# Optimization experiments

Hardware: AMD Instinct MI355X
Metric: run time of the kernel (lower is better)

## Reference

```python
import jax, jax.numpy as jnp
import numpy as np

IFZ = 256      # in_features
SFZ = 1280     # sequence_features
AHZ = 8        # attention heads
AFZ = 64       # attention feature dim per head
NRES = 20      # canonical_num_residues
SCALE = float(np.sqrt(AFZ))
RESID = float(np.sqrt(2.0))
EPS = 1e-6


def _ln(x, s, b, eps=1e-5):
    m = jnp.mean(x, axis=-1, keepdims=True)
    v = jnp.var(x, axis=-1, keepdims=True)
    return (x - m) / jnp.sqrt(v + eps) * s + b


def setup_inputs() -> dict:
    key = jax.random.key(0)
    ks = jax.random.split(key, 20)
    N, B, S = 4096, 4, 512
    HD = AHZ * AFZ
    w = lambda k, shp: (jax.random.normal(k, shp, jnp.float32) * 0.02)
    d = {}
    d["x"] = jax.random.normal(ks[0], (N, IFZ), jnp.float32)
    d["packed_sequence_emb"] = jax.random.normal(ks[1], (B, S, SFZ), jnp.float32)
    d["packed_sequence_mask"] = jnp.ones((B, S), jnp.float32)
    d["prot_mask"] = jnp.arange(N, dtype=jnp.int32)
    d["batch"] = jax.random.randint(ks[2], (N,), 0, B, jnp.int32)
    # projections (bias=False)
    d["Wq"] = w(ks[3], (HD, IFZ))
    d["Wk"] = w(ks[4], (HD, SFZ))
    d["Wv"] = w(ks[5], (HD, SFZ))
    # ag: LayerNorm(HD) -> Linear(HD, IFZ, bias=False) (dropout = identity at eval)
    d["ag_ln_s"] = jnp.ones((HD,), jnp.float32)
    d["ag_ln_b"] = jnp.zeros((HD,), jnp.float32)
    d["Wag"] = w(ks[6], (IFZ, HD))
    d["res_ln_s"] = jnp.ones((3, IFZ), jnp.float32)
    d["res_ln_b"] = jnp.zeros((3, IFZ), jnp.float32)
    d["res_w1"] = w(ks[7], (3, IFZ, IFZ))
    d["res_b1"] = jnp.zeros((3, IFZ), jnp.float32)
    d["res_w2"] = w(ks[8], (3, IFZ, IFZ))
    d["res_b2"] = jnp.zeros((3, IFZ), jnp.float32)
    d["head_w"] = w(ks[9], (NRES, IFZ))
    d["head_b"] = jnp.zeros((NRES,), jnp.float32)
    # output LayerNorm en
    d["en_s"] = jnp.ones((IFZ,), jnp.float32)
    d["en_b"] = jnp.zeros((IFZ,), jnp.float32)
    return d


def _forward(x, emb, mask, prot_mask, batch, Wq, Wk, Wv, ag_ln_s, ag_ln_b, Wag,
             res_ln_s, res_ln_b, res_w1, res_b1, res_w2, res_b2,
             head_w, head_b, en_s, en_b):
    N = x.shape[0]
    B, S = emb.shape[:2]
    b_idx = batch[prot_mask]                      # [M]
    xp = x[prot_mask]                             # [M, IFZ]
    M = xp.shape[0]
    q = (xp @ Wq.T).reshape(M, AHZ, AFZ)          # [M,H,D]
    k = (emb @ Wk.T).reshape(B, S, AHZ, AFZ)      # [B,S,H,D]
    v = (emb @ Wv.T).reshape(B, S, AHZ, AFZ)
    # score vs every protein, then pick own protein (avoids materializing [M,S,H,D] gather)
    scores_all = jnp.einsum('mhd,bshd->mbsh', q, k) / SCALE          # [M,B,S,H]
    sel = b_idx[:, None, None, None]
    scores = jnp.take_along_axis(scores_all, sel, axis=1)[:, 0]       # [M,S,H]
    mb = mask[b_idx][:, :, None]                                      # [M,S,1]
    # padded_sequence_softmax: softmax over S, zero pads, renormalize
    sm = jax.nn.softmax(scores, axis=1) * mb
    w = sm / (jnp.sum(sm, axis=1, keepdims=True) + EPS)               # [M,S,H]
    feat_all = jnp.einsum('msh,bshd->mbhd', w, v)                     # [M,B,H,D]
    feat = jnp.take_along_axis(feat_all, sel, axis=1)[:, 0]
    feat = feat.reshape(M, AHZ * AFZ)
    ag = _ln(feat, ag_ln_s, ag_ln_b) @ Wag.T                          # [M, IFZ]
    # seq_aa_head on the scattered new features (identical to ag for unique prot_mask)
    h = ag
    for i in range(3):
        y = _ln(h, res_ln_s[i], res_ln_b[i])
        y = jax.nn.relu(y @ res_w1[i].T + res_b1[i])
        y = y @ res_w2[i].T + res_b2[i]
        h = (h + y) / RESID
    logits = h @ head_w.T + head_b                                     # [M, NRES]
    new_features = jnp.zeros_like(x).at[prot_mask].set(ag)
    seq_aa_logits = jnp.zeros((N, NRES), x.dtype).at[prot_mask].set(logits)
    unpacked_scores = jnp.zeros((N, S, AHZ), x.dtype).at[prot_mask].set(scores)
    out_x = _ln(x + new_features / RESID, en_s, en_b)
    return out_x, seq_aa_logits, unpacked_scores


def reference(x, packed_sequence_emb, packed_sequence_mask, prot_mask, batch,
              Wq, Wk, Wv, ag_ln_s, ag_ln_b, Wag,
              res_ln_s, res_ln_b, res_w1, res_b1, res_w2, res_b2,
              head_w, head_b, en_s, en_b):
    return _forward(x, packed_sequence_emb, packed_sequence_mask, prot_mask, batch,
                    Wq, Wk, Wv, ag_ln_s, ag_ln_b, Wag,
                    res_ln_s, res_ln_b, res_w1, res_b1, res_w2, res_b2,
                    head_w, head_b, en_s, en_b)
```

## Files before the change

### kernel.cpp

```cpp
#include <hip/hip_runtime.h>
#include <math.h>


typedef short bf8 __attribute__((ext_vector_type(8)));
typedef float f32x4 __attribute__((ext_vector_type(4)));
typedef unsigned short u16;

constexpr int LDT = 40;
enum { EPI_NONE = 0, EPI_BIAS_RELU = 1, EPI_BIAS = 2, EPI_RESID = 3 };
#define RSQRT2 0.70710678118654752f

__device__ __forceinline__ u16 f2bf(float f) {
  unsigned int u = __builtin_bit_cast(unsigned int, f);
  unsigned int r = u + 0x7fffu + ((u >> 16) & 1u);
  return (u16)(r >> 16);
}
__device__ __forceinline__ float bf2f(u16 v) {
  return __builtin_bit_cast(float, (unsigned int)v << 16);
}
__device__ __forceinline__ f32x4 mfma16(bf8 a, bf8 b, f32x4 c) {
  return __builtin_amdgcn_mfma_f32_16x16x32_bf16(a, b, c, 0, 0, 0);
}

struct CvtDesc { const float* src; u16* dst; int n; };
struct CvtArgs { CvtDesc d[8]; };

__global__ __launch_bounds__(256) void cvt_k(CvtArgs a) {
  CvtDesc d = a.d[blockIdx.z];
  int i = (blockIdx.x * 256 + threadIdx.x) * 8;
  if (i >= d.n) return;
  f32x4 v0 = *(const f32x4*)(d.src + i);
  f32x4 v1 = *(const f32x4*)(d.src + i + 4);
  bf8 o;
  o[0] = (short)f2bf(v0[0]); o[1] = (short)f2bf(v0[1]);
  o[2] = (short)f2bf(v0[2]); o[3] = (short)f2bf(v0[3]);
  o[4] = (short)f2bf(v1[0]); o[5] = (short)f2bf(v1[1]);
  o[6] = (short)f2bf(v1[2]); o[7] = (short)f2bf(v1[3]);
  *(bf8*)(d.dst + i) = o;
}

template <int EPI, bool BFOUT>
__global__ __launch_bounds__(256) void mgemm2(
    const u16* __restrict__ A, const u16* __restrict__ B,
    void* __restrict__ Cv, int M, int N, int K, int lda, int ldb, int ldc,
    const float* __restrict__ bias, const float* __restrict__ Hin,
    const int* __restrict__ gatherA, const int* __restrict__ scatterC) {
  __shared__ __align__(16) u16 As[128 * LDT];
  __shared__ __align__(16) u16 Bs[64 * LDT];
  const int tid = threadIdx.x;
  const int m0 = blockIdx.y * 128, n0 = blockIdx.x * 64;
  const int wave = tid >> 6, lane = tid & 63;
  const int wm = (wave & 1) * 64, wn = (wave >> 1) * 32;
  const int lrow = lane & 15, quad = lane >> 4;
  const int srow = tid >> 2, skq = tid & 3;

  int gr0 = m0 + srow, gr1 = m0 + srow + 64;
  int ar0 = (gr0 < M) ? (gatherA ? gatherA[gr0] : gr0) : -1;
  int ar1 = (gr1 < M) ? (gatherA ? gatherA[gr1] : gr1) : -1;
  const u16* Ap0 = (ar0 >= 0) ? A + (size_t)ar0 * lda + skq * 8 : nullptr;
  const u16* Ap1 = (ar1 >= 0) ? A + (size_t)ar1 * lda + skq * 8 : nullptr;
  const u16* Bp = (n0 + srow < N) ? B + (size_t)(n0 + srow) * ldb + skq * 8 : nullptr;
  u16* AsW0 = &As[srow * LDT + skq * 8];
  u16* AsW1 = &As[(srow + 64) * LDT + skq * 8];
  u16* BsW = &Bs[srow * LDT + skq * 8];

  f32x4 acc[4][2];
#pragma unroll
  for (int i = 0; i < 4; ++i)
#pragma unroll
    for (int j = 0; j < 2; ++j) acc[i][j] = (f32x4){0.f, 0.f, 0.f, 0.f};
  const bf8 z8 = {0, 0, 0, 0, 0, 0, 0, 0};

  for (int k0 = 0; k0 < K; k0 += 32) {
    bf8 a0 = Ap0 ? *(const bf8*)(Ap0 + k0) : z8;
    bf8 a1 = Ap1 ? *(const bf8*)(Ap1 + k0) : z8;
    bf8 bv = Bp ? *(const bf8*)(Bp + k0) : z8;
    *(bf8*)AsW0 = a0;
    *(bf8*)AsW1 = a1;
    *(bf8*)BsW = bv;
    __syncthreads();
    bf8 af[4], bfr[2];
#pragma unroll
    for (int i = 0; i < 4; ++i)
      af[i] = *(const bf8*)&As[(wm + i * 16 + lrow) * LDT + quad * 8];
#pragma unroll
    for (int j = 0; j < 2; ++j)
      bfr[j] = *(const bf8*)&Bs[(wn + j * 16 + lrow) * LDT + quad * 8];
#pragma unroll
    for (int i = 0; i < 4; ++i)
#pragma unroll
      for (int j = 0; j < 2; ++j) acc[i][j] = mfma16(af[i], bfr[j], acc[i][j]);
    __syncthreads();
  }

  float* Cf = (float*)Cv;
  u16* Cb = (u16*)Cv;
#pragma unroll
  for (int i = 0; i < 4; ++i) {
#pragma unroll
    for (int r = 0; r < 4; ++r) {
      int row = m0 + wm + i * 16 + quad * 4 + r;
      if (row >= M) continue;
      if (gatherA && gatherA[row] < 0) continue;
      int orow = scatterC ? scatterC[row] : row;
#pragma unroll
      for (int j = 0; j < 2; ++j) {
        int col = n0 + wn + j * 16 + lrow;
        if (col >= N) continue;
        float v = acc[i][j][r];
        if (EPI == EPI_BIAS_RELU) v = fmaxf(v + bias[col], 0.f);
        else if (EPI == EPI_BIAS) v += bias[col];
        else if (EPI == EPI_RESID) v = (Hin[(size_t)row * ldc + col] + v + bias[col]) * RSQRT2;
        if (BFOUT) Cb[(size_t)orow * ldc + col] = f2bf(v);
        else Cf[(size_t)orow * ldc + col] = v;
      }
    }
  }
}

__global__ __launch_bounds__(256) void vtrans(const u16* __restrict__ KV,
                                              u16* __restrict__ VT) {
  __shared__ u16 t[32][33];
  int b = blockIdx.z;
  int s0 = blockIdx.x * 32, d0 = blockIdx.y * 32;
  int tx = threadIdx.x & 31, ty = threadIdx.x >> 5;
#pragma unroll
  for (int i = 0; i < 32; i += 8)
    t[ty + i][tx] = KV[(size_t)(b * 512 + s0 + ty + i) * 1024 + 512 + d0 + tx];
  __syncthreads();
#pragma unroll
  for (int i = 0; i < 32; i += 8)
    VT[(size_t)(b * 512 + d0 + ty + i) * 512 + s0 + tx] = t[tx][ty + i];
}

constexpr int WST = 520;
constexpr int QST = 72;

__global__ __launch_bounds__(256) void attn_fused(
    const u16* __restrict__ Q, const u16* __restrict__ KV,
    const u16* __restrict__ VT, const int* __restrict__ list,
    const float* __restrict__ mask, u16* __restrict__ packed,
    u16* __restrict__ feat, int N) {
  const int b = blockIdx.y >> 3, h = blockIdx.y & 7;
  const int mt = blockIdx.x;
  const int* lst = list + (size_t)b * N + mt * 32;
  if (lst[0] < 0) return;

  __shared__ __align__(16) u16 Ws[32 * WST];
  __shared__ __align__(16) u16 Qs[32 * QST];
  __shared__ __align__(16) u16 KVs[64 * QST];
  __shared__ __align__(16) float mk[8][68];
  __shared__ int mS[32];

  const int tid = threadIdx.x;
  const int wave = tid >> 6, lane = tid & 63;
  const int wm = (wave & 1) * 16, wns = (wave >> 1) * 32;
  const int lrow = lane & 15, quad = lane >> 4;
  const bf8 z8 = {0, 0, 0, 0, 0, 0, 0, 0};

  if (tid < 32) mS[tid] = lst[tid];
  {
    int p = tid >> 5, j = (tid & 31) * 2;
    *(float2*)&mk[p][j] = *(const float2*)&mask[(size_t)b * 512 + p * 64 + j];
  }
  {
    int qr = tid >> 3, kq = tid & 7;
    int m = lst[qr];
    *(bf8*)&Qs[qr * QST + kq * 8] =
        (m >= 0) ? *(const bf8*)(Q + (size_t)m * 512 + h * 64 + kq * 8) : z8;
  }
  __syncthreads();

  const bf8 qa0 = *(const bf8*)&Qs[(wm + lrow) * QST + 0 + quad * 8];
  const bf8 qa1 = *(const bf8*)&Qs[(wm + lrow) * QST + 32 + quad * 8];

  const u16* KVb = KV + (size_t)(b * 512) * 1024 + h * 64;
  for (int st = 0; st < 8; ++st) {
#pragma unroll
    for (int i = 0; i < 2; ++i) {
      int c = tid * 2 + i;
      int sr = c >> 3, kq = c & 7;
      *(bf8*)&KVs[sr * QST + kq * 8] =
          *(const bf8*)(KVb + (size_t)(st * 64 + sr) * 1024 + kq * 8);
    }
    __syncthreads();
    f32x4 acc0 = {0.f, 0.f, 0.f, 0.f}, acc1 = acc0;
    {
      bf8 b00 = *(const bf8*)&KVs[(wns + lrow) * QST + quad * 8];
      bf8 b10 = *(const bf8*)&KVs[(wns + 16 + lrow) * QST + quad * 8];
      bf8 b01 = *(const bf8*)&KVs[(wns + lrow) * QST + 32 + quad * 8];
      bf8 b11 = *(const bf8*)&KVs[(wns + 16 + lrow) * QST + 32 + quad * 8];
      acc0 = mfma16(qa0, b00, acc0);
      acc1 = mfma16(qa0, b10, acc1);
      acc0 = mfma16(qa1, b01, acc0);
      acc1 = mfma16(qa1, b11, acc1);
    }
#pragma unroll
    for (int r = 0; r < 4; ++r) {
      int lr = wm + quad * 4 + r;
      Ws[lr * WST + st * 64 + wns + lrow] = f2bf(acc0[r] * 0.125f);
      Ws[lr * WST + st * 64 + wns + 16 + lrow] = f2bf(acc1[r] * 0.125f);
    }
    __syncthreads();
  }

  {
    const int row = tid >> 3, part = tid & 7;
    u16* wrow = &Ws[row * WST + part * 64];
    const int mm = mS[row];
    bf8 w[8];
    float mx = -1e30f;
#pragma unroll
    for (int v = 0; v < 8; ++v) {
      w[v] = *(const bf8*)(wrow + v * 8);
#pragma unroll
      for (int j = 0; j < 8; ++j) mx = fmaxf(mx, bf2f((u16)w[v][j]));
    }
    if (mm >= 0) {
      u16* prow = packed + ((size_t)h * N + mm) * 512 + part * 64;
#pragma unroll
      for (int v = 0; v < 8; ++v) *(bf8*)(prow + v * 8) = w[v];
    }
#pragma unroll
    for (int d = 1; d < 8; d <<= 1) mx = fmaxf(mx, __shfl_xor(mx, d));
    float se = 0.f, ms = 0.f;
#pragma unroll
    for (int v = 0; v < 8; ++v) {
      f32x4 m0 = *(const f32x4*)&mk[part][v * 8];
      f32x4 m1 = *(const f32x4*)&mk[part][v * 8 + 4];
#pragma unroll
      for (int j = 0; j < 8; ++j) {
        float e = __expf(bf2f((u16)w[v][j]) - mx);
        se += e;
        ms += e * (j < 4 ? m0[j] : m1[j - 4]);
      }
    }
#pragma unroll
    for (int d = 1; d < 8; d <<= 1) {
      se += __shfl_xor(se, d);
      ms += __shfl_xor(ms, d);
    }
    float iv = 1.0f / (ms + 1e-6f * se);
#pragma unroll
    for (int v = 0; v < 8; ++v) {
      f32x4 m0 = *(const f32x4*)&mk[part][v * 8];
      f32x4 m1 = *(const f32x4*)&mk[part][v * 8 + 4];
      bf8 o;
#pragma unroll
      for (int j = 0; j < 8; ++j) {
        float e = __expf(bf2f((u16)w[v][j]) - mx);
        o[j] = (short)f2bf(e * (j < 4 ? m0[j] : m1[j - 4]) * iv);
      }
      *(bf8*)(wrow + v * 8) = o;
    }
  }
  __syncthreads();

  f32x4 acc0 = {0.f, 0.f, 0.f, 0.f}, acc1 = acc0;
  const u16* VTb = VT + (size_t)(b * 512 + h * 64) * 512;
  for (int s0 = 0; s0 < 512; s0 += 64) {
#pragma unroll
    for (int i = 0; i < 2; ++i) {
      int c = tid * 2 + i;
      int sr = c >> 3, kq = c & 7;
      *(bf8*)&KVs[sr * QST + kq * 8] =
          *(const bf8*)(VTb + (size_t)sr * 512 + s0 + kq * 8);
    }
    __syncthreads();
#pragma unroll
    for (int k0 = 0; k0 < 64; k0 += 32) {
      bf8 a = *(const bf8*)&Ws[(wm + lrow) * WST + s0 + k0 + quad * 8];
      bf8 b0 = *(const bf8*)&KVs[(wns + lrow) * QST + k0 + quad * 8];
      bf8 b1 = *(const bf8*)&KVs[(wns + 16 + lrow) * QST + k0 + quad * 8];
      acc0 = mfma16(a, b0, acc0);
      acc1 = mfma16(a, b1, acc1);
    }
    __syncthreads();
  }
#pragma unroll
  for (int r = 0; r < 4; ++r) {
    int lr = wm + quad * 4 + r;
    int mm = mS[lr];
    if (mm < 0) continue;
    u16* frow = feat + (size_t)mm * 512 + h * 64;
    frow[wns + lrow] = f2bf(acc0[r]);
    frow[wns + 16 + lrow] = f2bf(acc1[r]);
  }
}

__global__ __launch_bounds__(256) void unpack_k(const u16* __restrict__ packed,
                                                const int* __restrict__ pm,
                                                float* __restrict__ out_sc,
                                                int N) {
  __shared__ u16 Ls[8 * 520];
  int m = blockIdx.x, tid = threadIdx.x;
  int h = tid >> 5, c = (tid & 31) * 16;
  const u16* row = packed + ((size_t)h * N + m) * 512 + c;
  *(bf8*)&Ls[h * 520 + c] = *(const bf8*)row;
  *(bf8*)&Ls[h * 520 + c + 8] = *(const bf8*)(row + 8);
  __syncthreads();
  float* orow = out_sc + (size_t)pm[m] * 4096;
#pragma unroll
  for (int i = 0; i < 16; ++i) {
    int e = tid + i * 256;
    orow[e] = bf2f(Ls[(e & 7) * 520 + (e >> 3)]);
  }
}

constexpr int HST = 268;
constexpr int AST = 520;
constexpr int YST = 280;

__global__ __launch_bounds__(512) void mlp_fused(
    const u16* __restrict__ feat, const float* __restrict__ ag_s,
    const float* __restrict__ ag_b, const u16* __restrict__ Wag,
    float* __restrict__ AGout, const float* __restrict__ rls,
    const float* __restrict__ rlb, const u16* __restrict__ rw1,
    const float* __restrict__ rb1, const u16* __restrict__ rw2,
    const float* __restrict__ rb2, const float* __restrict__ hw,
    const float* __restrict__ hb, const int* __restrict__ pm,
    float* __restrict__ out_lg) {
  __shared__ __align__(16) float Hs[16 * HST];
  __shared__ __align__(16) u16 As[16 * AST];
  __shared__ __align__(16) u16 Ys[16 * YST];
  const int tid = threadIdx.x;
  const int m0 = blockIdx.x * 16;
  const int wave = tid >> 6, lane = tid & 63;
  const int lrow = lane & 15, quad = lane >> 4;
  const int wn = wave * 32;
  const int row = tid >> 5, part = tid & 31;

  {
    const u16* frow = feat + (size_t)(m0 + row) * 512 + part * 16;
    bf8 f0 = *(const bf8*)frow;
    bf8 f1 = *(const bf8*)(frow + 8);
    float s = 0.f, sq = 0.f;
#pragma unroll
    for (int j = 0; j < 8; ++j) {
      float a = bf2f((u16)f0[j]), b = bf2f((u16)f1[j]);
      s += a + b;
      sq += a * a + b * b;
    }
#pragma unroll
    for (int d = 1; d < 32; d <<= 1) { s += __shfl_xor(s, d); sq += __shfl_xor(sq, d); }
    float mean = s * (1.0f / 512.0f);
    float var = sq * (1.0f / 512.0f) - mean * mean;
    float is = 1.0f / sqrtf(var + 1e-5f);
    int c = part * 16;
    bf8 o0, o1;
#pragma unroll
    for (int j = 0; j < 8; ++j) {
      o0[j] = (short)f2bf((bf2f((u16)f0[j]) - mean) * is * ag_s[c + j] + ag_b[c + j]);
      o1[j] = (short)f2bf((bf2f((u16)f1[j]) - mean) * is * ag_s[c + 8 + j] + ag_b[c + 8 + j]);
    }
    *(bf8*)&As[row * AST + c] = o0;
    *(bf8*)&As[row * AST + c + 8] = o1;
  }
  __syncthreads();

  {
    f32x4 acc0 = {0.f, 0.f, 0.f, 0.f}, acc1 = acc0;
#pragma unroll 4
    for (int k0 = 0; k0 < 512; k0 += 32) {
      bf8 a = *(const bf8*)&As[lrow * AST + k0 + quad * 8];
      bf8 w0 = *(const bf8*)&Wag[(size_t)(wn + lrow) * 512 + k0 + quad * 8];
      bf8 w1 = *(const bf8*)&Wag[(size_t)(wn + 16 + lrow) * 512 + k0 + quad * 8];
      acc0 = mfma16(a, w0, acc0);
      acc1 = mfma16(a, w1, acc1);
    }
#pragma unroll
    for (int r = 0; r < 4; ++r) {
      int rr = quad * 4 + r;
      Hs[rr * HST + wn + lrow] = acc0[r];
      Hs[rr * HST + wn + 16 + lrow] = acc1[r];
      AGout[(size_t)(m0 + rr) * 256 + wn + lrow] = acc0[r];
      AGout[(size_t)(m0 + rr) * 256 + wn + 16 + lrow] = acc1[r];
    }
  }

  for (int layer = 0; layer < 3; ++layer) {
    __syncthreads();
    {
      int c = part * 8;
      f32x4 h0 = *(const f32x4*)&Hs[row * HST + c];
      f32x4 h1 = *(const f32x4*)&Hs[row * HST + c + 4];
      float s = 0.f, sq = 0.f;
#pragma unroll
      for (int e = 0; e < 4; ++e) {
        s += h0[e] + h1[e];
        sq += h0[e] * h0[e] + h1[e] * h1[e];
      }
#pragma unroll
      for (int d = 1; d < 32; d <<= 1) { s += __shfl_xor(s, d); sq += __shfl_xor(sq, d); }
      float mean = s * (1.0f / 256.0f);
      float var = sq * (1.0f / 256.0f) - mean * mean;
      float is = 1.0f / sqrtf(var + 1e-5f);
      const float* g = rls + layer * 256;
      const float* bb = rlb + layer * 256;
      bf8 o;
#pragma unroll
      for (int e = 0; e < 4; ++e) {
        o[e] = (short)f2bf((h0[e] - mean) * is * g[c + e] + bb[c + e]);
        o[e + 4] = (short)f2bf((h1[e] - mean) * is * g[c + 4 + e] + bb[c + 4 + e]);
      }
      *(bf8*)&As[row * AST + c] = o;
    }
    __syncthreads();

    {
      const u16* W = rw1 + (size_t)layer * 65536;
      f32x4 acc0 = {0.f, 0.f, 0.f, 0.f}, acc1 = acc0;
#pragma unroll 4
      for (int k0 = 0; k0 < 256; k0 += 32) {
        bf8 a = *(const bf8*)&As[lrow * AST + k0 + quad * 8];
        bf8 w0 = *(const bf8*)&W[(size_t)(wn + lrow) * 256 + k0 + quad * 8];
        bf8 w1 = *(const bf8*)&W[(size_t)(wn + 16 + lrow) * 256 + k0 + quad * 8];
        acc0 = mfma16(a, w0, acc0);
        acc1 = mfma16(a, w1, acc1);
      }
      const float* b1 = rb1 + layer * 256;
      float bi0 = b1[wn + lrow], bi1 = b1[wn + 16 + lrow];
#pragma unroll
      for (int r = 0; r < 4; ++r) {
        int rr = quad * 4 + r;
        Ys[rr * YST + wn + lrow] = f2bf(fmaxf(acc0[r] + bi0, 0.f));
        Ys[rr * YST + wn + 16 + lrow] = f2bf(fmaxf(acc1[r] + bi1, 0.f));
      }
    }
    __syncthreads();

    {
      const u16* W = rw2 + (size_t)layer * 65536;
      f32x4 acc0 = {0.f, 0.f, 0.f, 0.f}, acc1 = acc0;
#pragma unroll 4
      for (int k0 = 0; k0 < 256; k0 += 32) {
        bf8 a = *(const bf8*)&Ys[lrow * YST + k0 + quad * 8];
        bf8 w0 = *(const bf8*)&W[(size_t)(wn + lrow) * 256 + k0 + quad * 8];
        bf8 w1 = *(const bf8*)&W[(size_t)(wn + 16 + lrow) * 256 + k0 + quad * 8];
        acc0 = mfma16(a, w0, acc0);
        acc1 = mfma16(a, w1, acc1);
      }
      const float* b2 = rb2 + layer * 256;
      float bi0 = b2[wn + lrow], bi1 = b2[wn + 16 + lrow];
#pragma unroll
      for (int r = 0; r < 4; ++r) {
        int rr = quad * 4 + r;
        float* h0 = &Hs[rr * HST + wn + lrow];
        float* h1 = &Hs[rr * HST + wn + 16 + lrow];
        *h0 = (*h0 + acc0[r] + bi0) * RSQRT2;
        *h1 = (*h1 + acc1[r] + bi1) * RSQRT2;
      }
    }
  }
  __syncthreads();

  if (part < 20) {
    const float* hrow = &Hs[row * HST];
    const float* wrow = hw + (size_t)part * 256;
    float l0 = 0.f, l1 = 0.f, l2 = 0.f, l3 = 0.f;
    for (int k = 0; k < 256; k += 16) {
      f32x4 h0 = *(const f32x4*)&hrow[k];
      f32x4 h1 = *(const f32x4*)&hrow[k + 4];
      f32x4 h2 = *(const f32x4*)&hrow[k + 8];
      f32x4 h3 = *(const f32x4*)&hrow[k + 12];
      f32x4 w0 = *(const f32x4*)&wrow[k];
      f32x4 w1 = *(const f32x4*)&wrow[k + 4];
      f32x4 w2 = *(const f32x4*)&wrow[k + 8];
      f32x4 w3 = *(const f32x4*)&wrow[k + 12];
#pragma unroll
      for (int e = 0; e < 4; ++e) {
        l0 += h0[e] * w0[e];
        l1 += h1[e] * w1[e];
        l2 += h2[e] * w2[e];
        l3 += h3[e] * w3[e];
      }
    }
    out_lg[(size_t)pm[m0 + row] * 20 + part] = l0 + l1 + l2 + l3 + hb[part];
  }
}

__global__ __launch_bounds__(256) void outx_k(
    const float* __restrict__ x, const float* __restrict__ ag,
    const int* __restrict__ inv, const float* __restrict__ g,
    const float* __restrict__ bb, float* __restrict__ out) {
  __shared__ float red[256];
  int n = blockIdx.x, tid = threadIdx.x;
  int mi = inv[n];
  float v = x[(size_t)n * 256 + tid];
  if (mi >= 0) v += ag[(size_t)mi * 256 + tid] * RSQRT2;
  red[tid] = v;
  __syncthreads();
  for (int off = 128; off; off >>= 1) {
    if (tid < off) red[tid] += red[tid + off];
    __syncthreads();
  }
  float mean = red[0] * (1.0f / 256.0f);
  __syncthreads();
  red[tid] = v * v;
  __syncthreads();
  for (int off = 128; off; off >>= 1) {
    if (tid < off) red[tid] += red[tid + off];
    __syncthreads();
  }
  float var = red[0] * (1.0f / 256.0f) - mean * mean;
  float is = 1.0f / sqrtf(var + 1e-5f);
  out[(size_t)n * 256 + tid] = (v - mean) * is * g[tid] + bb[tid];
}

__global__ void init_idx_k(int* __restrict__ list, int* __restrict__ inv,
                           int* __restrict__ cnt, int N, int B) {
  int i = blockIdx.x * 256 + threadIdx.x;
  if (i < B * N) list[i] = -1;
  if (i < N) inv[i] = -1;
  if (i < B) cnt[i] = 0;
}

__global__ void compact_k(const int* __restrict__ pm,
                          const int* __restrict__ batch, int* __restrict__ list,
                          int* __restrict__ inv, int* __restrict__ cnt, int N) {
  int m = blockIdx.x * 256 + threadIdx.x;
  if (m >= N) return;
  int p = pm[m];
  int b = batch[p];
  int slot = atomicAdd(&cnt[b], 1);
  list[(size_t)b * N + slot] = m;
  inv[p] = m;
}

extern "C" void kernel_launch(void* const* d_in, const int* in_sizes, int n_in,
                              void* d_out, int out_size, void* d_ws,
                              size_t ws_size, hipStream_t stream) {
  const float* x = (const float*)d_in[0];
  const float* emb = (const float*)d_in[1];
  const float* mask = (const float*)d_in[2];
  const int* pm = (const int*)d_in[3];
  const int* batch = (const int*)d_in[4];
  const float* Wq = (const float*)d_in[5];
  const float* Wk = (const float*)d_in[6];
  const float* Wv = (const float*)d_in[7];
  const float* ag_s = (const float*)d_in[8];
  const float* ag_b = (const float*)d_in[9];
  const float* Wag = (const float*)d_in[10];
  const float* rls = (const float*)d_in[11];
  const float* rlb = (const float*)d_in[12];
  const float* rw1 = (const float*)d_in[13];
  const float* rb1 = (const float*)d_in[14];
  const float* rw2 = (const float*)d_in[15];
  const float* rb2 = (const float*)d_in[16];
  const float* hw = (const float*)d_in[17];
  const float* hb = (const float*)d_in[18];
  const float* ens = (const float*)d_in[19];
  const float* enb = (const float*)d_in[20];

  const int N = in_sizes[0] / 256;
  const int B = in_sizes[2] / 512;

  char* wsb = (char*)d_ws;
  u16* embbf = (u16*)(wsb + 0);
  u16* xbf   = (u16*)(wsb + 5242880);
  u16* Wkvbf = (u16*)(wsb + 7340032);
  u16* Wqbf  = (u16*)(wsb + 9961472);
  u16* packed = (u16*)(wsb + 0);
  u16* KVbf   = (u16*)(wsb + 33554432);
  u16* Qbf    = (u16*)(wsb + 37748736);
  u16* VT     = (u16*)(wsb + 41943040);
  u16* featE  = (u16*)(wsb + 44040192);
  float* AG = (float*)(wsb + 37748736);
  u16* Wagbf = (u16*)(wsb + 48234496);
  u16* rw1bf = (u16*)(wsb + 48496640);
  u16* rw2bf = (u16*)(wsb + 48889856);
  int* list  = (int*)(wsb + 49545216);
  int* inv   = (int*)(wsb + 49610752);
  int* cnt   = (int*)(wsb + 49627136);

  float* out_x = (float*)d_out;
  float* out_lg = out_x + (size_t)N * 256;
  float* out_sc = out_lg + (size_t)N * 20;

  CvtArgs ca;
  ca.d[0] = {emb, embbf, 2 * 512 * 1280 * 2};
  ca.d[1] = {x, xbf, 4096 * 256};
  ca.d[2] = {Wk, Wkvbf, 512 * 1280};
  ca.d[3] = {Wv, Wkvbf + 512 * 1280, 512 * 1280};
  ca.d[4] = {Wq, Wqbf, 512 * 256};
  ca.d[5] = {Wag, Wagbf, 256 * 512};
  ca.d[6] = {rw1, rw1bf, 3 * 256 * 256};
  ca.d[7] = {rw2, rw2bf, 3 * 256 * 256};
  cvt_k<<<dim3(1281, 1, 8), 256, 0, stream>>>(ca);
  init_idx_k<<<(B * N + 255) / 256, 256, 0, stream>>>(list, inv, cnt, N, B);
  compact_k<<<(N + 255) / 256, 256, 0, stream>>>(pm, batch, list, inv, cnt, N);

  mgemm2<EPI_NONE, true><<<dim3(16, 16), 256, 0, stream>>>(
      embbf, Wkvbf, KVbf, B * 512, 1024, 1280, 1280, 1280, 1024,
      nullptr, nullptr, nullptr, nullptr);
  mgemm2<EPI_NONE, true><<<dim3(8, 32), 256, 0, stream>>>(
      xbf, Wqbf, Qbf, N, 512, 256, 256, 256, 512,
      nullptr, nullptr, pm, nullptr);
  vtrans<<<dim3(16, 16, B), 256, 0, stream>>>(KVbf, VT);

  attn_fused<<<dim3(N / 32, B * 8), 256, 0, stream>>>(
      Qbf, KVbf, VT, list, mask, packed, featE, N);
  unpack_k<<<N, 256, 0, stream>>>(packed, pm, out_sc, N);

  mlp_fused<<<dim3(N / 16), 512, 0, stream>>>(
      featE, ag_s, ag_b, Wagbf, AG, rls, rlb, rw1bf, rb1, rw2bf, rb2,
      hw, hb, pm, out_lg);

  outx_k<<<N, 256, 0, stream>>>(x, AG, inv, ens, enb, out_x);
}
```

Before: 310.5 us.

## Halve MLP rows per block, rotate K-loop start per block, cache softmax exps

The MLP kernel now handles 8 real rows per block (the other 8 MFMA rows duplicate them) and launches twice as many blocks, so more CUs stay busy. Its K loops, and the attention kernel's K/V tile loops, start at a per-block rotated offset so concurrent blocks read different parts of the weights and K/V at once instead of all hitting the same addresses. The attention softmax stores its 64 exponentials in registers rather than computing them twice. Costs: half of each MFMA in the MLP does redundant work, and the 64-float array raises register pressure.

```diff
diff --git a/kernel.cpp b/kernel.cpp
--- a/kernel.cpp
+++ b/kernel.cpp
@@ -176,12 +176,13 @@
 
   const u16* KVb = KV + (size_t)(b * 512) * 1024 + h * 64;
   for (int st = 0; st < 8; ++st) {
+    const int sta = (st + mt) & 7;
 #pragma unroll
     for (int i = 0; i < 2; ++i) {
       int c = tid * 2 + i;
       int sr = c >> 3, kq = c & 7;
       *(bf8*)&KVs[sr * QST + kq * 8] =
-          *(const bf8*)(KVb + (size_t)(st * 64 + sr) * 1024 + kq * 8);
+          *(const bf8*)(KVb + (size_t)(sta * 64 + sr) * 1024 + kq * 8);
     }
     __syncthreads();
     f32x4 acc0 = {0.f, 0.f, 0.f, 0.f}, acc1 = acc0;
@@ -198,8 +199,8 @@
 #pragma unroll
     for (int r = 0; r < 4; ++r) {
       int lr = wm + quad * 4 + r;
-      Ws[lr * WST + st * 64 + wns + lrow] = f2bf(acc0[r] * 0.125f);
-      Ws[lr * WST + st * 64 + wns + 16 + lrow] = f2bf(acc1[r] * 0.125f);
+      Ws[lr * WST + sta * 64 + wns + lrow] = f2bf(acc0[r] * 0.125f);
+      Ws[lr * WST + sta * 64 + wns + 16 + lrow] = f2bf(acc1[r] * 0.125f);
     }
     __syncthreads();
   }
@@ -223,6 +224,7 @@
     }
 #pragma unroll
     for (int d = 1; d < 8; d <<= 1) mx = fmaxf(mx, __shfl_xor(mx, d));
+    float ev[64];
     float se = 0.f, ms = 0.f;
 #pragma unroll
     for (int v = 0; v < 8; ++v) {
@@ -231,6 +233,7 @@
 #pragma unroll
       for (int j = 0; j < 8; ++j) {
         float e = __expf(bf2f((u16)w[v][j]) - mx);
+        ev[v * 8 + j] = e;
         se += e;
         ms += e * (j < 4 ? m0[j] : m1[j - 4]);
       }
@@ -247,10 +250,8 @@
       f32x4 m1 = *(const f32x4*)&mk[part][v * 8 + 4];
       bf8 o;
 #pragma unroll
-      for (int j = 0; j < 8; ++j) {
-        float e = __expf(bf2f((u16)w[v][j]) - mx);
-        o[j] = (short)f2bf(e * (j < 4 ? m0[j] : m1[j - 4]) * iv);
-      }
+      for (int j = 0; j < 8; ++j)
+        o[j] = (short)f2bf(ev[v * 8 + j] * (j < 4 ? m0[j] : m1[j - 4]) * iv);
       *(bf8*)(wrow + v * 8) = o;
     }
   }
@@ -258,7 +259,8 @@
 
   f32x4 acc0 = {0.f, 0.f, 0.f, 0.f}, acc1 = acc0;
   const u16* VTb = VT + (size_t)(b * 512 + h * 64) * 512;
-  for (int s0 = 0; s0 < 512; s0 += 64) {
+  for (int ss = 0; ss < 8; ++ss) {
+    const int s0 = ((ss + mt) & 7) << 6;
 #pragma unroll
     for (int i = 0; i < 2; ++i) {
       int c = tid * 2 + i;
@@ -324,14 +326,15 @@
   __shared__ __align__(16) u16 As[16 * AST];
   __shared__ __align__(16) u16 Ys[16 * YST];
   const int tid = threadIdx.x;
-  const int m0 = blockIdx.x * 16;
+  const int m0 = blockIdx.x * 8;
   const int wave = tid >> 6, lane = tid & 63;
   const int lrow = lane & 15, quad = lane >> 4;
   const int wn = wave * 32;
   const int row = tid >> 5, part = tid & 31;
+  const int rot16 = blockIdx.x & 15, rot8 = blockIdx.x & 7;
 
   {
-    const u16* frow = feat + (size_t)(m0 + row) * 512 + part * 16;
+    const u16* frow = feat + (size_t)(m0 + (row & 7)) * 512 + part * 16;
     bf8 f0 = *(const bf8*)frow;
     bf8 f1 = *(const bf8*)(frow + 8);
     float s = 0.f, sq = 0.f;
@@ -361,7 +364,8 @@
   {
     f32x4 acc0 = {0.f, 0.f, 0.f, 0.f}, acc1 = acc0;
 #pragma unroll 4
-    for (int k0 = 0; k0 < 512; k0 += 32) {
+    for (int kk = 0; kk < 16; ++kk) {
+      int k0 = ((kk + rot16) & 15) << 5;
       bf8 a = *(const bf8*)&As[lrow * AST + k0 + quad * 8];
       bf8 w0 = *(const bf8*)&Wag[(size_t)(wn + lrow) * 512 + k0 + quad * 8];
       bf8 w1 = *(const bf8*)&Wag[(size_t)(wn + 16 + lrow) * 512 + k0 + quad * 8];
@@ -373,8 +377,10 @@
       int rr = quad * 4 + r;
       Hs[rr * HST + wn + lrow] = acc0[r];
       Hs[rr * HST + wn + 16 + lrow] = acc1[r];
-      AGout[(size_t)(m0 + rr) * 256 + wn + lrow] = acc0[r];
-      AGout[(size_t)(m0 + rr) * 256 + wn + 16 + lrow] = acc1[r];
+      if (rr < 8) {
+        AGout[(size_t)(m0 + rr) * 256 + wn + lrow] = acc0[r];
+        AGout[(size_t)(m0 + rr) * 256 + wn + 16 + lrow] = acc1[r];
+      }
     }
   }
 
@@ -411,7 +417,8 @@
       const u16* W = rw1 + (size_t)layer * 65536;
       f32x4 acc0 = {0.f, 0.f, 0.f, 0.f}, acc1 = acc0;
 #pragma unroll 4
-      for (int k0 = 0; k0 < 256; k0 += 32) {
+      for (int kk = 0; kk < 8; ++kk) {
+        int k0 = ((kk + rot8) & 7) << 5;
         bf8 a = *(const bf8*)&As[lrow * AST + k0 + quad * 8];
         bf8 w0 = *(const bf8*)&W[(size_t)(wn + lrow) * 256 + k0 + quad * 8];
         bf8 w1 = *(const bf8*)&W[(size_t)(wn + 16 + lrow) * 256 + k0 + quad * 8];
@@ -433,7 +440,8 @@
       const u16* W = rw2 + (size_t)layer * 65536;
       f32x4 acc0 = {0.f, 0.f, 0.f, 0.f}, acc1 = acc0;
 #pragma unroll 4
-      for (int k0 = 0; k0 < 256; k0 += 32) {
+      for (int kk = 0; kk < 8; ++kk) {
+        int k0 = ((kk + rot8) & 7) << 5;
         bf8 a = *(const bf8*)&Ys[lrow * YST + k0 + quad * 8];
         bf8 w0 = *(const bf8*)&W[(size_t)(wn + lrow) * 256 + k0 + quad * 8];
         bf8 w1 = *(const bf8*)&W[(size_t)(wn + 16 + lrow) * 256 + k0 + quad * 8];
@@ -454,7 +462,7 @@
   }
   __syncthreads();
 
-  if (part < 20) {
+  if (row < 8 && part < 20) {
     const float* hrow = &Hs[row * HST];
     const float* wrow = hw + (size_t)part * 256;
     float l0 = 0.f, l1 = 0.f, l2 = 0.f, l3 = 0.f;
@@ -602,7 +610,7 @@
       Qbf, KVbf, VT, list, mask, packed, featE, N);
   unpack_k<<<N, 256, 0, stream>>>(packed, pm, out_sc, N);
 
-  mlp_fused<<<dim3(N / 16), 512, 0, stream>>>(
+  mlp_fused<<<dim3(N / 8), 512, 0, stream>>>(
       featE, ag_s, ag_b, Wagbf, AG, rls, rlb, rw1bf, rb1, rw2bf, rb2,
       hw, hb, pm, out_lg);
 
```

New measurement: 336.8 us. +8.5%, slower.
